# Kernel optimization log

Hardware: AMD Instinct MI355X
Metric: run time of the kernel (lower is better)

The kernel has to match this reference:

```python
import jax, jax.numpy as jnp
import numpy as np

N, E, G = 50000, 800000, 128
IN, HID, OUT, H = 128, 64, 32, 4
EPS = 1e-5


def _bn(x, g, b, m, v):
    # BatchNorm1d in eval mode: normalize with running stats
    return (x - m) * jax.lax.rsqrt(v + EPS) * g + b


def _gat(x, src, dst, W, att_src, att_dst, bias, n):
    # PyG GATConv, concat=False: mean over heads
    h = (x @ W).reshape(n, H, -1)                      # [N,H,C]
    a_src = (h * att_src).sum(-1)                      # [N,H]
    a_dst = (h * att_dst).sum(-1)                      # [N,H]
    e = jax.nn.leaky_relu(a_src[src] + a_dst[dst], 0.2)  # [E,H]
    m = jax.ops.segment_max(e, dst, num_segments=n)    # segment softmax over incoming edges
    e = jnp.exp(e - m[dst])
    s = jax.ops.segment_sum(e, dst, num_segments=n)
    alpha = e / s[dst]                                  # [E,H]
    out = jax.ops.segment_sum(alpha[:, :, None] * h[src], dst, num_segments=n)  # [N,H,C]
    return out.mean(axis=1) + bias


def setup_inputs() -> dict:
    key = jax.random.key(0)
    ks = jax.random.split(key, 20)
    d = {
        "x": jax.random.normal(ks[0], (N, IN), jnp.float32),
        "edge_index": jax.random.randint(ks[1], (2, E), 0, N),
        "batch": jnp.sort(jax.random.randint(ks[2], (N,), 0, G)),
        # input_norm
        "in_gamma": jax.random.normal(ks[3], (IN,)) * 0.05 + 1.0,
        "in_beta": jax.random.normal(ks[4], (IN,)) * 0.05,
        "in_mean": jax.random.normal(ks[5], (IN,)) * 0.05,
        "in_var": jax.random.uniform(ks[6], (IN,)) + 0.5,
        # gat1
        "W1": jax.random.normal(ks[7], (IN, H * HID)) * (1.0 / np.sqrt(IN)),
        "as1": jax.random.normal(ks[8], (H, HID)) * 0.1,
        "ad1": jax.random.normal(ks[9], (H, HID)) * 0.1,
        "b1": jnp.zeros((HID,)),
        "bn1_g": jnp.ones((HID,)),
        "bn1_b": jnp.zeros((HID,)),
        "bn1_m": jax.random.normal(ks[10], (HID,)) * 0.05,
        "bn1_v": jax.random.uniform(ks[11], (HID,)) + 0.5,
        # gat2
        "W2": jax.random.normal(ks[12], (HID, H * HID)) * (1.0 / np.sqrt(HID)),
        "as2": jax.random.normal(ks[13], (H, HID)) * 0.1,
        "ad2": jax.random.normal(ks[14], (H, HID)) * 0.1,
        "b2": jnp.zeros((HID,)),
        "bn2_g": jnp.ones((HID,)),
        "bn2_b": jnp.zeros((HID,)),
        "bn2_m": jax.random.normal(ks[15], (HID,)) * 0.05,
        "bn2_v": jax.random.uniform(ks[16], (HID,)) + 0.5,
        # head
        "fc1_w": jax.random.normal(ks[17], (HID, HID // 2)) * (1.0 / np.sqrt(HID)),
        "fc1_b": jnp.zeros((HID // 2,)),
        "fc2_w": jax.random.normal(ks[18], (HID // 2, OUT)) * (1.0 / np.sqrt(HID // 2)),
        "fc2_b": jnp.zeros((OUT,)),
    }
    return d


def reference(x, edge_index, batch, in_gamma, in_beta, in_mean, in_var,
              W1, as1, ad1, b1, bn1_g, bn1_b, bn1_m, bn1_v,
              W2, as2, ad2, b2, bn2_g, bn2_b, bn2_m, bn2_v,
              fc1_w, fc1_b, fc2_w, fc2_b):
    n = x.shape[0]
    # PyG GATConv adds self-loops by default
    loop = jnp.arange(n)
    src = jnp.concatenate([edge_index[0], loop])
    dst = jnp.concatenate([edge_index[1], loop])

    h = _bn(x, in_gamma, in_beta, in_mean, in_var)
    h = _gat(h, src, dst, W1, as1, ad1, b1, n)
    h = jax.nn.relu(_bn(h, bn1_g, bn1_b, bn1_m, bn1_v))
    # dropout p=0.3 is identity in eval mode
    h = _gat(h, src, dst, W2, as2, ad2, b2, n)
    h = jax.nn.relu(_bn(h, bn2_g, bn2_b, bn2_m, bn2_v))

    # global mean pool over graphs
    sums = jax.ops.segment_sum(h, batch, num_segments=G)
    cnts = jax.ops.segment_sum(jnp.ones((n,), h.dtype), batch, num_segments=G)
    emb = sums / jnp.maximum(cnts, 1.0)[:, None]

    out = jax.nn.relu(emb @ fc1_w + fc1_b)
    return out @ fc2_w + fc2_b
```

## Files before the change

### kernel.cpp

```cpp
#include <hip/hip_runtime.h>
#include <hip/hip_bf16.h>

#define EPS   1e-5f
#define NH    4
#define DIN   128
#define DHID  64
#define DOUT  32
#define PNODES 256
#define CAP   128
#define GM    32
#define NBUCK 64
#define BSTR  16
#define EPT   16
#define EPB   (256 * EPT)

typedef __attribute__((ext_vector_type(8))) short short8;
typedef __attribute__((ext_vector_type(4))) float f32x4;
typedef __attribute__((ext_vector_type(2))) float f32x2;

__device__ __forceinline__ float us2f(unsigned short u) {
    return __uint_as_float((unsigned)u << 16);
}
__device__ __forceinline__ unsigned short f2us(float v) {
    __hip_bfloat16 hb = __float2bfloat16(v);
    return *(unsigned short*)&hb;
}
__device__ __forceinline__ unsigned char f2e4m3(float v) {
    int p = __builtin_amdgcn_cvt_pk_fp8_f32(v, 0.f, 0, false);
    return (unsigned char)(p & 0xff);
}
__device__ __forceinline__ float lrelu(float a) { return (a >= 0.f) ? a : 0.2f * a; }

__global__ void k_init0(int* __restrict__ deg, float* __restrict__ pool,
                        int* __restrict__ bcur, int N, int npool) {
    int g = blockIdx.x * blockDim.x + threadIdx.x;
    if (g < N) deg[g] = 1;
    if (g < npool) pool[g] = 0.f;
    if (g < NBUCK * BSTR) bcur[g] = 0;
}

__global__ __launch_bounds__(256) void k_scan_a(const int* __restrict__ deg,
                                                int* __restrict__ rowptr,
                                                int* __restrict__ bsum, int N) {
    __shared__ int sh[256];
    const int t = threadIdx.x;
    const int i = blockIdx.x * 256 + t;
    int v = (i < N) ? deg[i] : 0;
    sh[t] = v;
    __syncthreads();
    #pragma unroll
    for (int o = 1; o < 256; o <<= 1) {
        int u = (t >= o) ? sh[t - o] : 0;
        __syncthreads();
        sh[t] += u;
        __syncthreads();
    }
    if (i < N) rowptr[i] = sh[t] - v;
    if (t == 255) bsum[blockIdx.x] = sh[255];
}

__global__ __launch_bounds__(256) void k_scan_b(int* __restrict__ bsum, int nb) {
    __shared__ int sh[256];
    const int t = threadIdx.x;
    int v = (t < nb) ? bsum[t] : 0;
    sh[t] = v;
    __syncthreads();
    #pragma unroll
    for (int o = 1; o < 256; o <<= 1) {
        int u = (t >= o) ? sh[t - o] : 0;
        __syncthreads();
        sh[t] += u;
        __syncthreads();
    }
    if (t < nb) bsum[t] = sh[t] - v;
}

__global__ __launch_bounds__(256) void k_scan_c(int* __restrict__ rowptr,
                                                int* __restrict__ cursor,
                                                const int* __restrict__ bsum,
                                                int N, int Etot) {
    const int i = blockIdx.x * 256 + threadIdx.x;
    if (i < N) {
        int v = rowptr[i] + bsum[blockIdx.x];
        rowptr[i] = v;
        cursor[i] = v;
    }
    if (i == 0) rowptr[N] = Etot;
}

__global__ __launch_bounds__(256) void k_part(
    const int* __restrict__ ei, int E, int N, int bshift,
    unsigned long long* __restrict__ arena, int* __restrict__ bcur,
    int* __restrict__ deg, int cap)
{
    __shared__ int lhist[NBUCK];
    __shared__ int lbase[NBUCK];
    const int t = threadIdx.x;
    const int e0 = blockIdx.x * EPB;
    const int eEnd = min(e0 + EPB, E + N);

    if (t < NBUCK) lhist[t] = 0;
    __syncthreads();

    int myb[EPT], myd[EPT], mys[EPT];
    #pragma unroll
    for (int r = 0; r < EPT; ++r) {
        int e = e0 + r * 256 + t;
        myb[r] = -1;
        if (e < eEnd) {
            int s, d;
            if (e < E) { s = ei[e]; d = ei[E + e]; atomicAdd(&deg[d], 1); }
            else       { s = d = e - E; }
            int b = d >> bshift;
            myb[r] = b; myd[r] = d; mys[r] = s;
            atomicAdd(&lhist[b], 1);
        }
    }
    __syncthreads();

    if (t < NBUCK) {
        int c = lhist[t];
        lbase[t] = c ? atomicAdd(&bcur[t * BSTR], c) : 0;
        lhist[t] = 0;
    }
    __syncthreads();

    #pragma unroll
    for (int r = 0; r < EPT; ++r) {
        int b = myb[r];
        if (b >= 0) {
            int li = atomicAdd(&lhist[b], 1);
            int pos = lbase[b] + li;
            if (pos >= cap) pos = cap - 1;
            arena[(size_t)b * cap + pos] =
                ((unsigned long long)(unsigned)myd[r] << 32) | (unsigned)mys[r];
        }
    }
}

__global__ __launch_bounds__(256) void k_fill2(
    const unsigned long long* __restrict__ arena, const int* __restrict__ bcur,
    int cap, int* __restrict__ cursor, int* __restrict__ col)
{
    const int b = blockIdx.x;
    const int idx = blockIdx.y * 256 + threadIdx.x;
    if (idx >= bcur[b * BSTR]) return;
    unsigned long long v = arena[(size_t)b * cap + idx];
    int d = (int)(v >> 32);
    int s = (int)(v & 0xffffffffu);
    int pos = atomicAdd(&cursor[d], 1);
    col[pos] = s;
}

__global__ __launch_bounds__(256) void k_prepw(
    const float* __restrict__ ing, const float* __restrict__ inb,
    const float* __restrict__ inm, const float* __restrict__ inv,
    const float* __restrict__ W1, const float* __restrict__ W2,
    const float* __restrict__ as1, const float* __restrict__ ad1,
    const float* __restrict__ as2, const float* __restrict__ ad2,
    const float* __restrict__ b1,
    const float* __restrict__ bn1g, const float* __restrict__ bn1b,
    const float* __restrict__ bn1m, const float* __restrict__ bn1v,
    unsigned short* __restrict__ Wt, unsigned short* __restrict__ Wt2,
    unsigned short* __restrict__ Wast1, unsigned short* __restrict__ Wast2,
    float* __restrict__ scl1, float* __restrict__ shf1,
    float* __restrict__ sclX, float* __restrict__ shfX)
{
    int g = blockIdx.x * blockDim.x + threadIdx.x;
    if (g < 256 * DIN) {
        int n = g >> 7, k = g & 127;
        Wt[g] = f2us(W1[(size_t)k * 256 + n]);
    }
    if (g < 256 * DHID) {
        int n = g >> 6, k = g & 63;
        Wt2[g] = f2us(W2[(size_t)k * 256 + n]);
    }
    if (g < 16 * DIN) {
        int c = g >> 7, k = g & 127;
        float s = 0.f;
        if (c < 4)      { for (int j = 0; j < 64; ++j) s += W1[(size_t)k * 256 + c * 64 + j] * as1[c * 64 + j]; }
        else if (c < 8) { for (int j = 0; j < 64; ++j) s += W1[(size_t)k * 256 + (c - 4) * 64 + j] * ad1[(c - 4) * 64 + j]; }
        Wast1[g] = f2us(s);
    }
    if (g < 16 * DHID) {
        int c = g >> 6, k = g & 63;
        float s = 0.f;
        if (c < 4)      { for (int j = 0; j < 64; ++j) s += W2[(size_t)k * 256 + c * 64 + j] * as2[c * 64 + j]; }
        else if (c < 8) { for (int j = 0; j < 64; ++j) s += W2[(size_t)k * 256 + (c - 4) * 64 + j] * ad2[(c - 4) * 64 + j]; }
        Wast2[g] = f2us(s);
    }
    if (g < DHID) {
        float sc = bn1g[g] * rsqrtf(bn1v[g] + EPS);
        scl1[g] = sc;
        shf1[g] = (b1[g] - bn1m[g]) * sc + bn1b[g];
    }
    if (g < DIN) {
        float sc = ing[g] * rsqrtf(inv[g] + EPS);
        sclX[g] = sc;
        shfX[g] = inb[g] - inm[g] * sc;
    }
}

__global__ __launch_bounds__(256) void k_gemm1(
    const float* __restrict__ x,
    const float* __restrict__ sclX, const float* __restrict__ shfX,
    const unsigned short* __restrict__ Wt,
    const unsigned short* __restrict__ Wast,
    unsigned char* __restrict__ h,
    float* __restrict__ asrc, float* __restrict__ adst, int N)
{
    __shared__ float Csh[GM][260];
    const int t = threadIdx.x;
    const int lane = t & 63, wv = t >> 6;
    const int qm = lane & 15, qd = lane >> 4;
    const int base = blockIdx.x * GM;

    short8 afr[2][4];
    #pragma unroll
    for (int ks = 0; ks < 4; ++ks) {
        const int k0 = qd * 8 + ks * 32;
        float4 s0 = *(const float4*)(sclX + k0), s1 = *(const float4*)(sclX + k0 + 4);
        float4 h0 = *(const float4*)(shfX + k0), h1 = *(const float4*)(shfX + k0 + 4);
        #pragma unroll
        for (int rt = 0; rt < 2; ++rt) {
            int node = base + rt * 16 + qm;
            if (node >= N) node = N - 1;
            const float* xp = x + (size_t)node * DIN + k0;
            float4 x0 = *(const float4*)xp, x1 = *(const float4*)(xp + 4);
            short8 v;
            v[0] = f2us(x0.x * s0.x + h0.x); v[1] = f2us(x0.y * s0.y + h0.y);
            v[2] = f2us(x0.z * s0.z + h0.z); v[3] = f2us(x0.w * s0.w + h0.w);
            v[4] = f2us(x1.x * s1.x + h1.x); v[5] = f2us(x1.y * s1.y + h1.y);
            v[6] = f2us(x1.z * s1.z + h1.z); v[7] = f2us(x1.w * s1.w + h1.w);
            afr[rt][ks] = v;
        }
    }

    const int n0 = wv * 64;
    f32x4 acc[2][4];
    #pragma unroll
    for (int rt = 0; rt < 2; ++rt)
        #pragma unroll
        for (int ct = 0; ct < 4; ++ct)
            acc[rt][ct] = (f32x4){0.f, 0.f, 0.f, 0.f};

    #pragma unroll
    for (int ct = 0; ct < 4; ++ct) {
        const unsigned short* bp = Wt + (size_t)(n0 + ct * 16 + qm) * DIN + qd * 8;
        #pragma unroll
        for (int ks = 0; ks < 4; ++ks) {
            short8 bfr = *(const short8*)(bp + ks * 32);
            acc[0][ct] = __builtin_amdgcn_mfma_f32_16x16x32_bf16(afr[0][ks], bfr, acc[0][ct], 0, 0, 0);
            acc[1][ct] = __builtin_amdgcn_mfma_f32_16x16x32_bf16(afr[1][ks], bfr, acc[1][ct], 0, 0, 0);
// ... 87 lines not shown
    {
        const unsigned short* wp = Wast + (size_t)qm * DHID + qd * 8;
        f32x4 aat[2];
        aat[0] = (f32x4){0.f, 0.f, 0.f, 0.f};
        aat[1] = (f32x4){0.f, 0.f, 0.f, 0.f};
        #pragma unroll
        for (int ks = 0; ks < 2; ++ks) {
            short8 wfr = *(const short8*)(wp + ks * 32);
            aat[0] = __builtin_amdgcn_mfma_f32_16x16x32_bf16(afr[0][ks], wfr, aat[0], 0, 0, 0);
            aat[1] = __builtin_amdgcn_mfma_f32_16x16x32_bf16(afr[1][ks], wfr, aat[1], 0, 0, 0);
        }
        const int c = qm;
        #pragma unroll
        for (int rt = 0; rt < 2; ++rt)
            #pragma unroll
            for (int rg = 0; rg < 4; ++rg) {
                int nd = base + rt * 16 + qd * 4 + rg;
                if (nd < N) {
                    if (c < 4)      asrc[nd * 4 + c] = aat[rt][rg];
                    else if (c < 8) adst[nd * 4 + (c - 4)] = aat[rt][rg];
                }
            }
    }

    #pragma unroll
    for (int rt = 0; rt < 2; ++rt)
        #pragma unroll
        for (int ct = 0; ct < 4; ++ct)
            #pragma unroll
            for (int rg = 0; rg < 4; ++rg)
                Csh[rt * 16 + qd * 4 + rg][n0 + ct * 16 + qm] = acc[rt][ct][rg];
    __syncthreads();

    const int hcol = ((t & 3) << 6) | (t >> 2);
    for (int r = 0; r < GM; ++r) {
        int node = base + r;
        if (node >= N) break;
        h[(size_t)node * 256 + t] = f2e4m3(Csh[r][hcol]);
    }
}

__global__ __launch_bounds__(256) void k_agg(
    const int* __restrict__ rowptr, const int* __restrict__ col,
    const float* __restrict__ asrc, const float* __restrict__ adst,
    const unsigned char* __restrict__ h8,
    float* __restrict__ outf, unsigned short* __restrict__ outb,
    const float* __restrict__ scl, const float* __restrict__ shf,
    int mode, int N)
{
    __shared__ float4 exs[4][CAP];
    __shared__ int    cols[4][CAP];
    const int lane = threadIdx.x & 63;
    const int wv   = threadIdx.x >> 6;
    const int d = (blockIdx.x << 2) + wv;
    if (d >= N) return;
    const int r0  = rowptr[d];
    const int deg = rowptr[d + 1] - r0;

    const float4 ad4 = ((const float4*)adst)[d];
    const float4* __restrict__ as4 = (const float4*)asrc;

    float sm0 = 0.f, sm1 = 0.f, sm2 = 0.f, sm3 = 0.f;
    for (int j = lane; j < deg; j += 64) {
        int s = col[r0 + j];
        float4 a = as4[s];
        float e0 = __expf(lrelu(a.x + ad4.x));
        float e1 = __expf(lrelu(a.y + ad4.y));
        float e2 = __expf(lrelu(a.z + ad4.z));
        float e3 = __expf(lrelu(a.w + ad4.w));
        if (j < CAP) { cols[wv][j] = s; exs[wv][j] = make_float4(e0, e1, e2, e3); }
        sm0 += e0; sm1 += e1; sm2 += e2; sm3 += e3;
    }
    #pragma unroll
    for (int o = 1; o < 64; o <<= 1) {
        sm0 += __shfl_xor(sm0, o, 64);
        sm1 += __shfl_xor(sm1, o, 64);
        sm2 += __shfl_xor(sm2, o, 64);
        sm3 += __shfl_xor(sm3, o, 64);
    }
    const float i0 = 0.25f / sm0, i1 = 0.25f / sm1, i2 = 0.25f / sm2, i3 = 0.25f / sm3;

    const unsigned int* __restrict__ hu = (const unsigned int*)h8;
    float a0 = 0.f, a1 = 0.f, a2 = 0.f, a3 = 0.f;
    float b0 = 0.f, b1 = 0.f, b2 = 0.f, b3 = 0.f;
    if (deg <= CAP) {
        int j = 0;
        for (; j + 3 < deg; j += 4) {
            int sA = cols[wv][j],     sB = cols[wv][j + 1];
            int sC = cols[wv][j + 2], sD = cols[wv][j + 3];
            unsigned int vA = hu[(size_t)sA * 64 + lane];
            unsigned int vB = hu[(size_t)sB * 64 + lane];
            unsigned int vC = hu[(size_t)sC * 64 + lane];
            unsigned int vD = hu[(size_t)sD * 64 + lane];
            float4 wA = exs[wv][j],     wB = exs[wv][j + 1];
            float4 wC = exs[wv][j + 2], wD = exs[wv][j + 3];
            f32x2 lA = __builtin_amdgcn_cvt_pk_f32_fp8(vA, false), hA = __builtin_amdgcn_cvt_pk_f32_fp8(vA, true);
            f32x2 lB = __builtin_amdgcn_cvt_pk_f32_fp8(vB, false), hB = __builtin_amdgcn_cvt_pk_f32_fp8(vB, true);
            f32x2 lC = __builtin_amdgcn_cvt_pk_f32_fp8(vC, false), hC = __builtin_amdgcn_cvt_pk_f32_fp8(vC, true);
            f32x2 lD = __builtin_amdgcn_cvt_pk_f32_fp8(vD, false), hD = __builtin_amdgcn_cvt_pk_f32_fp8(vD, true);
            a0 += wA.x * lA.x; a1 += wA.y * lA.y; a2 += wA.z * hA.x; a3 += wA.w * hA.y;
            b0 += wB.x * lB.x; b1 += wB.y * lB.y; b2 += wB.z * hB.x; b3 += wB.w * hB.y;
            a0 += wC.x * lC.x; a1 += wC.y * lC.y; a2 += wC.z * hC.x; a3 += wC.w * hC.y;
            b0 += wD.x * lD.x; b1 += wD.y * lD.y; b2 += wD.z * hD.x; b3 += wD.w * hD.y;
        }
        for (; j < deg; ++j) {
            int s = cols[wv][j];
            unsigned int v = hu[(size_t)s * 64 + lane];
            float4 w = exs[wv][j];
            f32x2 lo = __builtin_amdgcn_cvt_pk_f32_fp8(v, false), hi = __builtin_amdgcn_cvt_pk_f32_fp8(v, true);
            a0 += w.x * lo.x; a1 += w.y * lo.y; a2 += w.z * hi.x; a3 += w.w * hi.y;
        }
    } else {
        for (int j = 0; j < deg; ++j) {
            int s; float4 w;
            if (j < CAP) { s = cols[wv][j]; w = exs[wv][j]; }
            else {
                s = col[r0 + j];
                float4 a = as4[s];
                w.x = __expf(lrelu(a.x + ad4.x)); w.y = __expf(lrelu(a.y + ad4.y));
                w.z = __expf(lrelu(a.z + ad4.z)); w.w = __expf(lrelu(a.w + ad4.w));
            }
            unsigned int v = hu[(size_t)s * 64 + lane];
            f32x2 lo = __builtin_amdgcn_cvt_pk_f32_fp8(v, false), hi = __builtin_amdgcn_cvt_pk_f32_fp8(v, true);
            a0 += w.x * lo.x; a1 += w.y * lo.y; a2 += w.z * hi.x; a3 += w.w * hi.y;
        }
    }
    float acc = (a0 + b0) * i0 + (a1 + b1) * i1 + (a2 + b2) * i2 + (a3 + b3) * i3;

    if (mode) {
        float v = fmaxf(acc * scl[lane] + shf[lane], 0.f);
        outb[(size_t)d * 64 + lane] = f2us(v);
    } else {
        outf[(size_t)d * 64 + lane] = acc;
    }
}

__global__ __launch_bounds__(256) void k_pool(
    const float* __restrict__ outacc,
    const float* __restrict__ b2_,
    const float* __restrict__ bg, const float* __restrict__ bb,
    const float* __restrict__ bm, const float* __restrict__ bv,
    const int* __restrict__ batch,
    float* __restrict__ pool, float* __restrict__ cnt, int N)
{
    const int lane = threadIdx.x & 63;
    const int wave = threadIdx.x >> 6;
    const int base = blockIdx.x * PNODES;
    int end = base + PNODES; if (end > N) end = N;

    const float scale = bg[lane] * rsqrtf(bv[lane] + EPS);
    const float shift = (b2_[lane] - bm[lane]) * scale + bb[lane];

    float acc = 0.f;
    int cur = -1, cl = 0;
    for (int n = base + wave; n < end; n += 4) {
        int gr = batch[n];
        if (gr != cur) {
            if (cur >= 0) {
                atomicAdd(&pool[cur * 64 + lane], acc);
                if (lane == 0) atomicAdd(&cnt[cur], (float)cl);
            }
            cur = gr; acc = 0.f; cl = 0;
        }
        float v = fmaxf(outacc[(size_t)n * 64 + lane] * scale + shift, 0.f);
        acc += v; ++cl;
    }
    if (cur >= 0) {
        atomicAdd(&pool[cur * 64 + lane], acc);
        if (lane == 0) atomicAdd(&cnt[cur], (float)cl);
    }
}

__global__ void k_head(const float* __restrict__ pool, const float* __restrict__ cnt,
                       const float* __restrict__ fc1w, const float* __restrict__ fc1b,
                       const float* __restrict__ fc2w, const float* __restrict__ fc2b,
                       float* __restrict__ out)
{
    int g = blockIdx.x;
    int t = threadIdx.x;
    __shared__ float emb[64];
    __shared__ float z1[32];
    float c = fmaxf(cnt[g], 1.0f);
    emb[t] = pool[g * 64 + t] / c;
    __syncthreads();
    if (t < 32) {
        float s = fc1b[t];
        for (int k = 0; k < 64; ++k) s += emb[k] * fc1w[k * 32 + t];
        z1[t] = fmaxf(s, 0.f);
    }
    __syncthreads();
    if (t < 32) {
        float o = fc2b[t];
        for (int j = 0; j < 32; ++j) o += z1[j] * fc2w[j * 32 + t];
        out[g * 32 + t] = o;
    }
}

extern "C" void kernel_launch(void* const* d_in, const int* in_sizes, int n_in,
                              void* d_out, int out_size, void* d_ws, size_t ws_size,
                              hipStream_t stream)
{
    const float* x    = (const float*)d_in[0];
    const int*   ei   = (const int*)d_in[1];
    const int*   batch= (const int*)d_in[2];
    const float* ing  = (const float*)d_in[3];
    const float* inb  = (const float*)d_in[4];
    const float* inm  = (const float*)d_in[5];
    const float* inv  = (const float*)d_in[6];
    const float* W1   = (const float*)d_in[7];
    const float* as1  = (const float*)d_in[8];
    const float* ad1  = (const float*)d_in[9];
    const float* b1   = (const float*)d_in[10];
    const float* bn1g = (const float*)d_in[11];
    const float* bn1b = (const float*)d_in[12];
    const float* bn1m = (const float*)d_in[13];
    const float* bn1v = (const float*)d_in[14];
    const float* W2   = (const float*)d_in[15];
    const float* as2  = (const float*)d_in[16];
    const float* ad2  = (const float*)d_in[17];
    const float* b2   = (const float*)d_in[18];
    const float* bn2g = (const float*)d_in[19];
    const float* bn2b = (const float*)d_in[20];
    const float* bn2m = (const float*)d_in[21];
    const float* bn2v = (const float*)d_in[22];
    const float* fc1w = (const float*)d_in[23];
    const float* fc1b = (const float*)d_in[24];
    const float* fc2w = (const float*)d_in[25];
    const float* fc2b = (const float*)d_in[26];

    const int N = in_sizes[0] / DIN;
    const int E = in_sizes[1] / 2;
    const int G = out_size / DOUT;
    const int Etot = E + N;

    int bshift = 0;
    while ((N >> bshift) >= NBUCK) ++bshift;
    const int cap = (int)(((long long)Etot << bshift) / N * 5 / 4) + 512;

    unsigned char* h8 = (unsigned char*)d_ws;
    float* asrc   = (float*)(h8 + (size_t)N * 256);
    float* adst   = asrc + (size_t)N * NH;
    unsigned short* Wt    = (unsigned short*)(adst + (size_t)N * NH);
    unsigned short* Wt2   = Wt + 256 * DIN;
    unsigned short* Wast1 = Wt2 + 256 * DHID;
    unsigned short* Wast2 = Wast1 + 16 * DIN;
    float* scl1   = (float*)(Wast2 + 16 * DHID);
    float* shf1   = scl1 + DHID;
    float* sclX   = shf1 + DHID;
    float* shfX   = sclX + DIN;
    float* outacc = shfX + DIN;
    unsigned short* A2 = (unsigned short*)outacc;
    int*   deg    = (int*)(outacc + (size_t)N * DHID);
    int*   rowptr = deg + N;
    int*   cursor = rowptr + N + 1;
    int*   col    = cursor + N;
    float* pool   = (float*)(col + Etot);
    float* cnt    = pool + (size_t)G * DHID;
    int*   bsum   = (int*)(cnt + G);
    int*   bcur   = (int*)(((size_t)(bsum + 256) + 63) & ~(size_t)63);
    unsigned long long* arena =
        (unsigned long long*)(((size_t)(bcur + NBUCK * BSTR) + 7) & ~(size_t)7);

    const int npool = G * DHID + G;
    const int nScanBlk = (N + 255) / 256;
    dim3 b256(256);

    k_init0<<<(N + 255) / 256, b256, 0, stream>>>(deg, pool, bcur, N, npool);
    k_part<<<(Etot + EPB - 1) / EPB, b256, 0, stream>>>(ei, E, N, bshift, arena, bcur, deg, cap);
    k_scan_a<<<nScanBlk, b256, 0, stream>>>(deg, rowptr, bsum, N);
    k_scan_b<<<1, b256, 0, stream>>>(bsum, nScanBlk);
    k_scan_c<<<nScanBlk, b256, 0, stream>>>(rowptr, cursor, bsum, N, Etot);
    {
        dim3 gFill(NBUCK, (cap + 255) / 256);
        k_fill2<<<gFill, b256, 0, stream>>>(arena, bcur, cap, cursor, col);
    }

    k_prepw<<<(256 * DIN + 255) / 256, b256, 0, stream>>>(
        ing, inb, inm, inv, W1, W2, as1, ad1, as2, ad2,
        b1, bn1g, bn1b, bn1m, bn1v,
        Wt, Wt2, Wast1, Wast2, scl1, shf1, sclX, shfX);

    k_gemm1<<<(N + GM - 1) / GM, b256, 0, stream>>>(x, sclX, shfX, Wt, Wast1, h8, asrc, adst, N);
    k_agg<<<(N + 3) / 4, b256, 0, stream>>>(rowptr, col, asrc, adst, h8,
                                            (float*)nullptr, A2, scl1, shf1, 1, N);

    k_gemm2<<<(N + GM - 1) / GM, b256, 0, stream>>>(A2, Wt2, Wast2, h8, asrc, adst, N);
    k_agg<<<(N + 3) / 4, b256, 0, stream>>>(rowptr, col, asrc, adst, h8,
                                            outacc, (unsigned short*)nullptr,
                                            (const float*)nullptr, (const float*)nullptr, 0, N);

    k_pool<<<(N + PNODES - 1) / PNODES, b256, 0, stream>>>(outacc, b2, bn2g, bn2b, bn2m, bn2v,
                                                           batch, pool, cnt, N);
    k_head<<<G, 64, 0, stream>>>(pool, cnt, fc1w, fc1b, fc2w, fc2b, (float*)d_out);
}
```

Before: 364.4 us.

## Handle self-loops implicitly, merge init/prep kernels, use 16-byte gathers in aggregation

Self-loop edges are no longer stored in the CSR. Each destination's self term is computed directly in the aggregation kernel and appended to the per-wave shared edge list. The init and weight-prep kernels are fused into one setup kernel to cut a launch. The aggregation gather is reorganized so 16-lane groups each load a full 256-byte fp8 row with uint4 loads, processing four edges per iteration and reducing across groups with shuffles; this widens memory transactions at the cost of more registers and a cross-group reduction.

```diff
diff --git a/kernel.cpp b/kernel.cpp
--- a/kernel.cpp
+++ b/kernel.cpp
@@ -31,128 +31,9 @@
 }
 __device__ __forceinline__ float lrelu(float a) { return (a >= 0.f) ? a : 0.2f * a; }
 
-__global__ void k_init0(int* __restrict__ deg, float* __restrict__ pool,
-                        int* __restrict__ bcur, int N, int npool) {
-    int g = blockIdx.x * blockDim.x + threadIdx.x;
-    if (g < N) deg[g] = 1;
-    if (g < npool) pool[g] = 0.f;
-    if (g < NBUCK * BSTR) bcur[g] = 0;
-}
-
-__global__ __launch_bounds__(256) void k_scan_a(const int* __restrict__ deg,
-                                                int* __restrict__ rowptr,
-                                                int* __restrict__ bsum, int N) {
-    __shared__ int sh[256];
-    const int t = threadIdx.x;
-    const int i = blockIdx.x * 256 + t;
-    int v = (i < N) ? deg[i] : 0;
-    sh[t] = v;
-    __syncthreads();
-    #pragma unroll
-    for (int o = 1; o < 256; o <<= 1) {
-        int u = (t >= o) ? sh[t - o] : 0;
-        __syncthreads();
-        sh[t] += u;
-        __syncthreads();
-    }
-    if (i < N) rowptr[i] = sh[t] - v;
-    if (t == 255) bsum[blockIdx.x] = sh[255];
-}
-
-__global__ __launch_bounds__(256) void k_scan_b(int* __restrict__ bsum, int nb) {
-    __shared__ int sh[256];
-    const int t = threadIdx.x;
-    int v = (t < nb) ? bsum[t] : 0;
-    sh[t] = v;
-    __syncthreads();
-    #pragma unroll
-    for (int o = 1; o < 256; o <<= 1) {
-        int u = (t >= o) ? sh[t - o] : 0;
-        __syncthreads();
-        sh[t] += u;
-        __syncthreads();
-    }
-    if (t < nb) bsum[t] = sh[t] - v;
-}
-
-__global__ __launch_bounds__(256) void k_scan_c(int* __restrict__ rowptr,
-                                                int* __restrict__ cursor,
-                                                const int* __restrict__ bsum,
-                                                int N, int Etot) {
-    const int i = blockIdx.x * 256 + threadIdx.x;
-    if (i < N) {
-        int v = rowptr[i] + bsum[blockIdx.x];
-        rowptr[i] = v;
-        cursor[i] = v;
-    }
-    if (i == 0) rowptr[N] = Etot;
-}
-
-__global__ __launch_bounds__(256) void k_part(
-    const int* __restrict__ ei, int E, int N, int bshift,
-    unsigned long long* __restrict__ arena, int* __restrict__ bcur,
-    int* __restrict__ deg, int cap)
-{
-    __shared__ int lhist[NBUCK];
-    __shared__ int lbase[NBUCK];
-    const int t = threadIdx.x;
-    const int e0 = blockIdx.x * EPB;
-    const int eEnd = min(e0 + EPB, E + N);
-
-    if (t < NBUCK) lhist[t] = 0;
-    __syncthreads();
-
-    int myb[EPT], myd[EPT], mys[EPT];
-    #pragma unroll
-    for (int r = 0; r < EPT; ++r) {
-        int e = e0 + r * 256 + t;
-        myb[r] = -1;
-        if (e < eEnd) {
-            int s, d;
-            if (e < E) { s = ei[e]; d = ei[E + e]; atomicAdd(&deg[d], 1); }
-            else       { s = d = e - E; }
-            int b = d >> bshift;
-            myb[r] = b; myd[r] = d; mys[r] = s;
-            atomicAdd(&lhist[b], 1);
-        }
-    }
-    __syncthreads();
-
-    if (t < NBUCK) {
-        int c = lhist[t];
-        lbase[t] = c ? atomicAdd(&bcur[t * BSTR], c) : 0;
-        lhist[t] = 0;
-    }
-    __syncthreads();
-
-    #pragma unroll
-    for (int r = 0; r < EPT; ++r) {
-        int b = myb[r];
-        if (b >= 0) {
-            int li = atomicAdd(&lhist[b], 1);
-            int pos = lbase[b] + li;
-            if (pos >= cap) pos = cap - 1;
-            arena[(size_t)b * cap + pos] =
-                ((unsigned long long)(unsigned)myd[r] << 32) | (unsigned)mys[r];
-        }
-    }
-}
-
-__global__ __launch_bounds__(256) void k_fill2(
-    const unsigned long long* __restrict__ arena, const int* __restrict__ bcur,
-    int cap, int* __restrict__ cursor, int* __restrict__ col)
-{
-    const int b = blockIdx.x;
-    const int idx = blockIdx.y * 256 + threadIdx.x;
-    if (idx >= bcur[b * BSTR]) return;
-    unsigned long long v = arena[(size_t)b * cap + idx];
-    int d = (int)(v >> 32);
-    int s = (int)(v & 0xffffffffu);
-    int pos = atomicAdd(&cursor[d], 1);
-    col[pos] = s;
-}
-
-__global__ __launch_bounds__(256) void k_prepw(
+__global__ __launch_bounds__(256) void k_setup(
+    int* __restrict__ deg, float* __restrict__ pool, int* __restrict__ bcur,
+    int N, int npool,
     const float* __restrict__ ing, const float* __restrict__ inb,
     const float* __restrict__ inm, const float* __restrict__ inv,
     const float* __restrict__ W1, const float* __restrict__ W2,
@@ -167,6 +48,9 @@
     float* __restrict__ sclX, float* __restrict__ shfX)
 {
     int g = blockIdx.x * blockDim.x + threadIdx.x;
+    if (g < N) deg[g] = 0;
+    if (g < npool) pool[g] = 0.f;
+    if (g < NBUCK * BSTR) bcur[g] = 0;
     if (g < 256 * DIN) {
         int n = g >> 7, k = g & 127;
         Wt[g] = f2us(W1[(size_t)k * 256 + n]);
@@ -199,6 +83,118 @@
         sclX[g] = sc;
         shfX[g] = inb[g] - inm[g] * sc;
     }
+}
+
+__global__ __launch_bounds__(256) void k_scan_a(const int* __restrict__ deg,
+                                                int* __restrict__ rowptr,
+                                                int* __restrict__ bsum, int N) {
+    __shared__ int sh[256];
+    const int t = threadIdx.x;
+    const int i = blockIdx.x * 256 + t;
+    int v = (i < N) ? deg[i] : 0;
+    sh[t] = v;
+    __syncthreads();
+    #pragma unroll
+    for (int o = 1; o < 256; o <<= 1) {
+        int u = (t >= o) ? sh[t - o] : 0;
+        __syncthreads();
+        sh[t] += u;
+        __syncthreads();
+    }
+    if (i < N) rowptr[i] = sh[t] - v;
+    if (t == 255) bsum[blockIdx.x] = sh[255];
+}
+
+__global__ __launch_bounds__(256) void k_scan_b(int* __restrict__ bsum, int nb) {
+    __shared__ int sh[256];
+    const int t = threadIdx.x;
+    int v = (t < nb) ? bsum[t] : 0;
+    sh[t] = v;
+    __syncthreads();
+    #pragma unroll
+    for (int o = 1; o < 256; o <<= 1) {
+        int u = (t >= o) ? sh[t - o] : 0;
+        __syncthreads();
+        sh[t] += u;
+        __syncthreads();
+    }
+    if (t < nb) bsum[t] = sh[t] - v;
+}
+
+__global__ __launch_bounds__(256) void k_scan_c(int* __restrict__ rowptr,
+                                                int* __restrict__ cursor,
+                                                const int* __restrict__ bsum,
+                                                int N, int Etot) {
+    const int i = blockIdx.x * 256 + threadIdx.x;
+    if (i < N) {
+        int v = rowptr[i] + bsum[blockIdx.x];
+        rowptr[i] = v;
+        cursor[i] = v;
+    }
+    if (i == 0) rowptr[N] = Etot;
+}
+
+__global__ __launch_bounds__(256) void k_part(
+    const int* __restrict__ ei, int E, int bshift,
+    unsigned long long* __restrict__ arena, int* __restrict__ bcur,
+    int* __restrict__ deg, int cap)
+{
+    __shared__ int lhist[NBUCK];
+    __shared__ int lbase[NBUCK];
+    const int t = threadIdx.x;
+    const int e0 = blockIdx.x * EPB;
+    const int eEnd = min(e0 + EPB, E);
+
+    if (t < NBUCK) lhist[t] = 0;
+    __syncthreads();
+
+    int myb[EPT], myd[EPT], mys[EPT];
+    #pragma unroll
+    for (int r = 0; r < EPT; ++r) {
+        int e = e0 + r * 256 + t;
+        myb[r] = -1;
+        if (e < eEnd) {
+            int s = ei[e], d = ei[E + e];
+            atomicAdd(&deg[d], 1);
+            int b = d >> bshift;
+            myb[r] = b; myd[r] = d; mys[r] = s;
+            atomicAdd(&lhist[b], 1);
+        }
+    }
+    __syncthreads();
+
+    if (t < NBUCK) {
+        int c = lhist[t];
+        lbase[t] = c ? atomicAdd(&bcur[t * BSTR], c) : 0;
+        lhist[t] = 0;
+    }
+    __syncthreads();
+
+    #pragma unroll
+    for (int r = 0; r < EPT; ++r) {
+        int b = myb[r];
+        if (b >= 0) {
+            int li = atomicAdd(&lhist[b], 1);
+            int pos = lbase[b] + li;
+            if (pos >= cap) pos = cap - 1;
+            arena[(size_t)b * cap + pos] =
+                ((unsigned long long)(unsigned)myd[r] << 32) | (unsigned)mys[r];
+        }
+    }
+}
+
+__global__ __launch_bounds__(256) void k_fill2(
+    const unsigned long long* __restrict__ arena, const int* __restrict__ bcur,
+    int cap, int* __restrict__ cursor, int* __restrict__ col)
+{
+    const int b = blockIdx.x;
+    const int idx = blockIdx.y * 256 + threadIdx.x;
+    if (idx >= bcur[b * BSTR]) return;
+    unsigned long long v = arena[(size_t)b * cap + idx];
+    int d = (int)(v >> 32);
+    int s = (int)(v & 0xffffffffu);
+    int pos = atomicAdd(&cursor[d], 1);
+    col[pos] = s;
 }
 
 __global__ __launch_bounds__(256) void k_gemm1(
@@ -392,13 +388,22 @@
     __shared__ int    cols[4][CAP];
     const int lane = threadIdx.x & 63;
     const int wv   = threadIdx.x >> 6;
+    const int grp  = lane >> 4;
+    const int l16  = lane & 15;
     const int d = (blockIdx.x << 2) + wv;
     if (d >= N) return;
     const int r0  = rowptr[d];
     const int deg = rowptr[d + 1] - r0;
+    const int degv = deg + 1;
 
     const float4 ad4 = ((const float4*)adst)[d];
     const float4* __restrict__ as4 = (const float4*)asrc;
+
+    const float4 a_s = as4[d];
+    const float ws0 = __expf(lrelu(a_s.x + ad4.x));
+    const float ws1 = __expf(lrelu(a_s.y + ad4.y));
+    const float ws2 = __expf(lrelu(a_s.z + ad4.z));
+    const float ws3 = __expf(lrelu(a_s.w + ad4.w));
 
     float sm0 = 0.f, sm1 = 0.f, sm2 = 0.f, sm3 = 0.f;
     for (int j = lane; j < deg; j += 64) {
@@ -418,60 +423,119 @@
         sm2 += __shfl_xor(sm2, o, 64);
         sm3 += __shfl_xor(sm3, o, 64);
     }
+    sm0 += ws0; sm1 += ws1; sm2 += ws2; sm3 += ws3;
     const float i0 = 0.25f / sm0, i1 = 0.25f / sm1, i2 = 0.25f / sm2, i3 = 0.25f / sm3;
 
-    const unsigned int* __restrict__ hu = (const unsigned int*)h8;
-    float a0 = 0.f, a1 = 0.f, a2 = 0.f, a3 = 0.f;
-    float b0 = 0.f, b1 = 0.f, b2 = 0.f, b3 = 0.f;
-    if (deg <= CAP) {
-        int j = 0;
-        for (; j + 3 < deg; j += 4) {
-            int sA = cols[wv][j],     sB = cols[wv][j + 1];
-            int sC = cols[wv][j + 2], sD = cols[wv][j + 3];
-            unsigned int vA = hu[(size_t)sA * 64 + lane];
-            unsigned int vB = hu[(size_t)sB * 64 + lane];
-            unsigned int vC = hu[(size_t)sC * 64 + lane];
-            unsigned int vD = hu[(size_t)sD * 64 + lane];
-            float4 wA = exs[wv][j],     wB = exs[wv][j + 1];
-            float4 wC = exs[wv][j + 2], wD = exs[wv][j + 3];
-            f32x2 lA = __builtin_amdgcn_cvt_pk_f32_fp8(vA, false), hA = __builtin_amdgcn_cvt_pk_f32_fp8(vA, true);
-            f32x2 lB = __builtin_amdgcn_cvt_pk_f32_fp8(vB, false), hB = __builtin_amdgcn_cvt_pk_f32_fp8(vB, true);
-            f32x2 lC = __builtin_amdgcn_cvt_pk_f32_fp8(vC, false), hC = __builtin_amdgcn_cvt_pk_f32_fp8(vC, true);
-            f32x2 lD = __builtin_amdgcn_cvt_pk_f32_fp8(vD, false), hD = __builtin_amdgcn_cvt_pk_f32_fp8(vD, true);
-            a0 += wA.x * lA.x; a1 += wA.y * lA.y; a2 += wA.z * hA.x; a3 += wA.w * hA.y;
-            b0 += wB.x * lB.x; b1 += wB.y * lB.y; b2 += wB.z * hB.x; b3 += wB.w * hB.y;
-            a0 += wC.x * lC.x; a1 += wC.y * lC.y; a2 += wC.z * hC.x; a3 += wC.w * hC.y;
-            b0 += wD.x * lD.x; b1 += wD.y * lD.y; b2 += wD.z * hD.x; b3 += wD.w * hD.y;
-        }
-        for (; j < deg; ++j) {
-            int s = cols[wv][j];
-            unsigned int v = hu[(size_t)s * 64 + lane];
-            float4 w = exs[wv][j];
-            f32x2 lo = __builtin_amdgcn_cvt_pk_f32_fp8(v, false), hi = __builtin_amdgcn_cvt_pk_f32_fp8(v, true);
-            a0 += w.x * lo.x; a1 += w.y * lo.y; a2 += w.z * hi.x; a3 += w.w * hi.y;
+    if (deg < CAP && lane == 0) {
+        cols[wv][deg] = d;
+        exs[wv][deg] = make_float4(ws0, ws1, ws2, ws3);
+    }
+
+    float acc[4][4];
+    #pragma unroll
+    for (int i = 0; i < 4; ++i)
+        #pragma unroll
+        for (int hh = 0; hh < 4; ++hh) acc[i][hh] = 0.f;
+
+    if (degv <= CAP) {
+        for (int j = 0; j < degv; j += 4) {
+            int e = j + grp;
+            int s = d;
+            float4 w = make_float4(0.f, 0.f, 0.f, 0.f);
+            if (e < degv) { s = cols[wv][e]; w = exs[wv][e]; }
+            uint4 v4 = *(const uint4*)(h8 + (size_t)s * 256 + l16 * 16);
+            {
+                f32x2 lo = __builtin_amdgcn_cvt_pk_f32_fp8(v4.x, false);
+                f32x2 hi = __builtin_amdgcn_cvt_pk_f32_fp8(v4.x, true);
+                acc[0][0] += w.x * lo.x; acc[0][1] += w.y * lo.y;
+                acc[0][2] += w.z * hi.x; acc[0][3] += w.w * hi.y;
+            }
+            {
+                f32x2 lo = __builtin_amdgcn_cvt_pk_f32_fp8(v4.y, false);
+                f32x2 hi = __builtin_amdgcn_cvt_pk_f32_fp8(v4.y, true);
+                acc[1][0] += w.x * lo.x; acc[1][1] += w.y * lo.y;
+                acc[1][2] += w.z * hi.x; acc[1][3] += w.w * hi.y;
+            }
+            {
+                f32x2 lo = __builtin_amdgcn_cvt_pk_f32_fp8(v4.z, false);
+                f32x2 hi = __builtin_amdgcn_cvt_pk_f32_fp8(v4.z, true);
+                acc[2][0] += w.x * lo.x; acc[2][1] += w.y * lo.y;
+                acc[2][2] += w.z * hi.x; acc[2][3] += w.w * hi.y;
+            }
+            {
+                f32x2 lo = __builtin_amdgcn_cvt_pk_f32_fp8(v4.w, false);
+                f32x2 hi = __builtin_amdgcn_cvt_pk_f32_fp8(v4.w, true);
+                acc[3][0] += w.x * lo.x; acc[3][1] += w.y * lo.y;
+                acc[3][2] += w.z * hi.x; acc[3][3] += w.w * hi.y;
+            }
         }
     } else {
-        for (int j = 0; j < deg; ++j) {
-            int s; float4 w;
-            if (j < CAP) { s = cols[wv][j]; w = exs[wv][j]; }
-            else {
-                s = col[r0 + j];
+        for (int j = 0; j < degv; j += 4) {
+            int e = j + grp;
+            int s = d;
+            float4 w = make_float4(0.f, 0.f, 0.f, 0.f);
+            if (e < CAP)      { s = cols[wv][e]; w = exs[wv][e]; }
+            else if (e < deg) {
+                s = col[r0 + e];
                 float4 a = as4[s];
                 w.x = __expf(lrelu(a.x + ad4.x)); w.y = __expf(lrelu(a.y + ad4.y));
                 w.z = __expf(lrelu(a.z + ad4.z)); w.w = __expf(lrelu(a.w + ad4.w));
             }
-            unsigned int v = hu[(size_t)s * 64 + lane];
-            f32x2 lo = __builtin_amdgcn_cvt_pk_f32_fp8(v, false), hi = __builtin_amdgcn_cvt_pk_f32_fp8(v, true);
-            a0 += w.x * lo.x; a1 += w.y * lo.y; a2 += w.z * hi.x; a3 += w.w * hi.y;
-        }
-    }
-    float acc = (a0 + b0) * i0 + (a1 + b1) * i1 + (a2 + b2) * i2 + (a3 + b3) * i3;
-
-    if (mode) {
-        float v = fmaxf(acc * scl[lane] + shf[lane], 0.f);
-        outb[(size_t)d * 64 + lane] = f2us(v);
-    } else {
-        outf[(size_t)d * 64 + lane] = acc;
+            else if (e == deg) { s = d; w = make_float4(ws0, ws1, ws2, ws3); }
+            uint4 v4 = *(const uint4*)(h8 + (size_t)s * 256 + l16 * 16);
+            {
+                f32x2 lo = __builtin_amdgcn_cvt_pk_f32_fp8(v4.x, false);
+                f32x2 hi = __builtin_amdgcn_cvt_pk_f32_fp8(v4.x, true);
+                acc[0][0] += w.x * lo.x; acc[0][1] += w.y * lo.y;
+                acc[0][2] += w.z * hi.x; acc[0][3] += w.w * hi.y;
+            }
+            {
+                f32x2 lo = __builtin_amdgcn_cvt_pk_f32_fp8(v4.y, false);
+                f32x2 hi = __builtin_amdgcn_cvt_pk_f32_fp8(v4.y, true);
+                acc[1][0] += w.x * lo.x; acc[1][1] += w.y * lo.y;
+                acc[1][2] += w.z * hi.x; acc[1][3] += w.w * hi.y;
+            }
+            {
+                f32x2 lo = __builtin_amdgcn_cvt_pk_f32_fp8(v4.z, false);
+                f32x2 hi = __builtin_amdgcn_cvt_pk_f32_fp8(v4.z, true);
+                acc[2][0] += w.x * lo.x; acc[2][1] += w.y * lo.y;
+                acc[2][2] += w.z * hi.x; acc[2][3] += w.w * hi.y;
+            }
+            {
+                f32x2 lo = __builtin_amdgcn_cvt_pk_f32_fp8(v4.w, false);
+                f32x2 hi = __builtin_amdgcn_cvt_pk_f32_fp8(v4.w, true);
+                acc[3][0] += w.x * lo.x; acc[3][1] += w.y * lo.y;
+                acc[3][2] += w.z * hi.x; acc[3][3] += w.w * hi.y;
+            }
+        }
+    }
+
+    float4 r;
+    {
+        float v0 = acc[0][0] * i0 + acc[0][1] * i1 + acc[0][2] * i2 + acc[0][3] * i3;
+        float v1 = acc[1][0] * i0 + acc[1][1] * i1 + acc[1][2] * i2 + acc[1][3] * i3;
+        float v2 = acc[2][0] * i0 + acc[2][1] * i1 + acc[2][2] * i2 + acc[2][3] * i3;
+        float v3 = acc[3][0] * i0 + acc[3][1] * i1 + acc[3][2] * i2 + acc[3][3] * i3;
+        v0 += __shfl_xor(v0, 16, 64); v0 += __shfl_xor(v0, 32, 64);
+        v1 += __shfl_xor(v1, 16, 64); v1 += __shfl_xor(v1, 32, 64);
+        v2 += __shfl_xor(v2, 16, 64); v2 += __shfl_xor(v2, 32, 64);
+        v3 += __shfl_xor(v3, 16, 64); v3 += __shfl_xor(v3, 32, 64);
+        r = make_float4(v0, v1, v2, v3);
+    }
+    if (grp == 0) {
+        const int c0 = l16 * 4;
+        if (mode) {
+            float4 sc = *(const float4*)(scl + c0);
+            float4 sf = *(const float4*)(shf + c0);
+            ushort4 o;
+            o.x = f2us(fmaxf(r.x * sc.x + sf.x, 0.f));
+            o.y = f2us(fmaxf(r.y * sc.y + sf.y, 0.f));
+            o.z = f2us(fmaxf(r.z * sc.z + sf.z, 0.f));
+            o.w = f2us(fmaxf(r.w * sc.w + sf.w, 0.f));
+            *(ushort4*)(outb + (size_t)d * 64 + c0) = o;
+        } else {
+            *(float4*)(outf + (size_t)d * 64 + c0) = r;
+        }
     }
 }
 
@@ -571,11 +635,10 @@
     const int N = in_sizes[0] / DIN;
     const int E = in_sizes[1] / 2;
     const int G = out_size / DOUT;
-    const int Etot = E + N;
 
     int bshift = 0;
     while ((N >> bshift) >= NBUCK) ++bshift;
-    const int cap = (int)(((long long)Etot << bshift) / N * 5 / 4) + 512;
+    const int cap = (int)(((long long)E << bshift) / N * 5 / 4) + 512;
 
     unsigned char* h8 = (unsigned char*)d_ws;
     float* asrc   = (float*)(h8 + (size_t)N * 256);
@@ -594,7 +657,7 @@
     int*   rowptr = deg + N;
     int*   cursor = rowptr + N + 1;
     int*   col    = cursor + N;
-    float* pool   = (float*)(col + Etot);
+    float* pool   = (float*)(col + E);
     float* cnt    = pool + (size_t)G * DHID;
     int*   bsum   = (int*)(cnt + G);
     int*   bcur   = (int*)(((size_t)(bsum + 256) + 63) & ~(size_t)63);
@@ -605,20 +668,23 @@
     const int nScanBlk = (N + 255) / 256;
     dim3 b256(256);
 
-    k_init0<<<(N + 255) / 256, b256, 0, stream>>>(deg, pool, bcur, N, npool);
-    k_part<<<(Etot + EPB - 1) / EPB, b256, 0, stream>>>(ei, E, N, bshift, arena, bcur, deg, cap);
+    int setupTot = N;
+    if (setupTot < npool) setupTot = npool;
+    if (setupTot < 256 * DIN) setupTot = 256 * DIN;
+    k_setup<<<(setupTot + 255) / 256, b256, 0, stream>>>(
+        deg, pool, bcur, N, npool,
+        ing, inb, inm, inv, W1, W2, as1, ad1, as2, ad2,
+        b1, bn1g, bn1b, bn1m, bn1v,
+        Wt, Wt2, Wast1, Wast2, scl1, shf1, sclX, shfX);
+
+    k_part<<<(E + EPB - 1) / EPB, b256, 0, stream>>>(ei, E, bshift, arena, bcur, deg, cap);
     k_scan_a<<<nScanBlk, b256, 0, stream>>>(deg, rowptr, bsum, N);
     k_scan_b<<<1, b256, 0, stream>>>(bsum, nScanBlk);
-    k_scan_c<<<nScanBlk, b256, 0, stream>>>(rowptr, cursor, bsum, N, Etot);
+    k_scan_c<<<nScanBlk, b256, 0, stream>>>(rowptr, cursor, bsum, N, E);
     {
         dim3 gFill(NBUCK, (cap + 255) / 256);
         k_fill2<<<gFill, b256, 0, stream>>>(arena, bcur, cap, cursor, col);
     }
-
-    k_prepw<<<(256 * DIN + 255) / 256, b256, 0, stream>>>(
-        ing, inb, inm, inv, W1, W2, as1, ad1, as2, ad2,
-        b1, bn1g, bn1b, bn1m, bn1v,
-        Wt, Wt2, Wast1, Wast2, scl1, shf1, sclX, shfX);
 
     k_gemm1<<<(N + GM - 1) / GM, b256, 0, stream>>>(x, sclX, shfX, Wt, Wast1, h8, asrc, adst, N);
     k_agg<<<(N + 3) / 4, b256, 0, stream>>>(rowptr, col, asrc, adst, h8,
```

Measured after the change: 373.5 us. 1.03x slower.

## Handle self-loops implicitly in aggregation and merge init with weight prep

Applied to the files above, without the earlier changes.

Self-loop edges are no longer built into the CSR. Degrees start at zero, the partition, scan and fill steps handle only the E real edges, and each aggregation wave computes the self-loop weight directly and appends it to its shared-memory neighbor list. The init kernel is also folded into the weight-preparation kernel, which removes one launch. This trims N entries from the CSR build and its atomics, in exchange for extra per-node work and extra branches in the aggregation kernel.

```diff
diff --git a/kernel.cpp b/kernel.cpp
--- a/kernel.cpp
+++ b/kernel.cpp
@@ -31,128 +31,9 @@
 }
 __device__ __forceinline__ float lrelu(float a) { return (a >= 0.f) ? a : 0.2f * a; }
 
-__global__ void k_init0(int* __restrict__ deg, float* __restrict__ pool,
-                        int* __restrict__ bcur, int N, int npool) {
-    int g = blockIdx.x * blockDim.x + threadIdx.x;
-    if (g < N) deg[g] = 1;
-    if (g < npool) pool[g] = 0.f;
-    if (g < NBUCK * BSTR) bcur[g] = 0;
-}
-
-__global__ __launch_bounds__(256) void k_scan_a(const int* __restrict__ deg,
-                                                int* __restrict__ rowptr,
-                                                int* __restrict__ bsum, int N) {
-    __shared__ int sh[256];
-    const int t = threadIdx.x;
-    const int i = blockIdx.x * 256 + t;
-    int v = (i < N) ? deg[i] : 0;
-    sh[t] = v;
-    __syncthreads();
-    #pragma unroll
-    for (int o = 1; o < 256; o <<= 1) {
-        int u = (t >= o) ? sh[t - o] : 0;
-        __syncthreads();
-        sh[t] += u;
-        __syncthreads();
-    }
-    if (i < N) rowptr[i] = sh[t] - v;
-    if (t == 255) bsum[blockIdx.x] = sh[255];
-}
-
-__global__ __launch_bounds__(256) void k_scan_b(int* __restrict__ bsum, int nb) {
-    __shared__ int sh[256];
-    const int t = threadIdx.x;
-    int v = (t < nb) ? bsum[t] : 0;
-    sh[t] = v;
-    __syncthreads();
-    #pragma unroll
-    for (int o = 1; o < 256; o <<= 1) {
-        int u = (t >= o) ? sh[t - o] : 0;
-        __syncthreads();
-        sh[t] += u;
-        __syncthreads();
-    }
-    if (t < nb) bsum[t] = sh[t] - v;
-}
-
-__global__ __launch_bounds__(256) void k_scan_c(int* __restrict__ rowptr,
-                                                int* __restrict__ cursor,
-                                                const int* __restrict__ bsum,
-                                                int N, int Etot) {
-    const int i = blockIdx.x * 256 + threadIdx.x;
-    if (i < N) {
-        int v = rowptr[i] + bsum[blockIdx.x];
-        rowptr[i] = v;
-        cursor[i] = v;
-    }
-    if (i == 0) rowptr[N] = Etot;
-}
-
-__global__ __launch_bounds__(256) void k_part(
-    const int* __restrict__ ei, int E, int N, int bshift,
-    unsigned long long* __restrict__ arena, int* __restrict__ bcur,
-    int* __restrict__ deg, int cap)
-{
-    __shared__ int lhist[NBUCK];
-    __shared__ int lbase[NBUCK];
-    const int t = threadIdx.x;
-    const int e0 = blockIdx.x * EPB;
-    const int eEnd = min(e0 + EPB, E + N);
-
-    if (t < NBUCK) lhist[t] = 0;
-    __syncthreads();
-
-    int myb[EPT], myd[EPT], mys[EPT];
-    #pragma unroll
-    for (int r = 0; r < EPT; ++r) {
-        int e = e0 + r * 256 + t;
-        myb[r] = -1;
-        if (e < eEnd) {
-            int s, d;
-            if (e < E) { s = ei[e]; d = ei[E + e]; atomicAdd(&deg[d], 1); }
-            else       { s = d = e - E; }
-            int b = d >> bshift;
-            myb[r] = b; myd[r] = d; mys[r] = s;
-            atomicAdd(&lhist[b], 1);
-        }
-    }
-    __syncthreads();
-
-    if (t < NBUCK) {
-        int c = lhist[t];
-        lbase[t] = c ? atomicAdd(&bcur[t * BSTR], c) : 0;
-        lhist[t] = 0;
-    }
-    __syncthreads();
-
-    #pragma unroll
-    for (int r = 0; r < EPT; ++r) {
-        int b = myb[r];
-        if (b >= 0) {
-            int li = atomicAdd(&lhist[b], 1);
-            int pos = lbase[b] + li;
-            if (pos >= cap) pos = cap - 1;
-            arena[(size_t)b * cap + pos] =
-                ((unsigned long long)(unsigned)myd[r] << 32) | (unsigned)mys[r];
-        }
-    }
-}
-
-__global__ __launch_bounds__(256) void k_fill2(
-    const unsigned long long* __restrict__ arena, const int* __restrict__ bcur,
-    int cap, int* __restrict__ cursor, int* __restrict__ col)
-{
-    const int b = blockIdx.x;
-    const int idx = blockIdx.y * 256 + threadIdx.x;
-    if (idx >= bcur[b * BSTR]) return;
-    unsigned long long v = arena[(size_t)b * cap + idx];
-    int d = (int)(v >> 32);
-    int s = (int)(v & 0xffffffffu);
-    int pos = atomicAdd(&cursor[d], 1);
-    col[pos] = s;
-}
-
-__global__ __launch_bounds__(256) void k_prepw(
+__global__ __launch_bounds__(256) void k_setup(
+    int* __restrict__ deg, float* __restrict__ pool, int* __restrict__ bcur,
+    int N, int npool,
     const float* __restrict__ ing, const float* __restrict__ inb,
     const float* __restrict__ inm, const float* __restrict__ inv,
     const float* __restrict__ W1, const float* __restrict__ W2,
@@ -167,6 +48,9 @@
     float* __restrict__ sclX, float* __restrict__ shfX)
 {
     int g = blockIdx.x * blockDim.x + threadIdx.x;
+    if (g < N) deg[g] = 0;
+    if (g < npool) pool[g] = 0.f;
+    if (g < NBUCK * BSTR) bcur[g] = 0;
     if (g < 256 * DIN) {
         int n = g >> 7, k = g & 127;
         Wt[g] = f2us(W1[(size_t)k * 256 + n]);
@@ -199,6 +83,118 @@
         sclX[g] = sc;
         shfX[g] = inb[g] - inm[g] * sc;
     }
+}
+
+__global__ __launch_bounds__(256) void k_scan_a(const int* __restrict__ deg,
+                                                int* __restrict__ rowptr,
+                                                int* __restrict__ bsum, int N) {
+    __shared__ int sh[256];
+    const int t = threadIdx.x;
+    const int i = blockIdx.x * 256 + t;
+    int v = (i < N) ? deg[i] : 0;
+    sh[t] = v;
+    __syncthreads();
+    #pragma unroll
+    for (int o = 1; o < 256; o <<= 1) {
+        int u = (t >= o) ? sh[t - o] : 0;
+        __syncthreads();
+        sh[t] += u;
+        __syncthreads();
+    }
+    if (i < N) rowptr[i] = sh[t] - v;
+    if (t == 255) bsum[blockIdx.x] = sh[255];
+}
+
+__global__ __launch_bounds__(256) void k_scan_b(int* __restrict__ bsum, int nb) {
+    __shared__ int sh[256];
+    const int t = threadIdx.x;
+    int v = (t < nb) ? bsum[t] : 0;
+    sh[t] = v;
+    __syncthreads();
+    #pragma unroll
+    for (int o = 1; o < 256; o <<= 1) {
+        int u = (t >= o) ? sh[t - o] : 0;
+        __syncthreads();
+        sh[t] += u;
+        __syncthreads();
+    }
+    if (t < nb) bsum[t] = sh[t] - v;
+}
+
+__global__ __launch_bounds__(256) void k_scan_c(int* __restrict__ rowptr,
+                                                int* __restrict__ cursor,
+                                                const int* __restrict__ bsum,
+                                                int N, int Etot) {
+    const int i = blockIdx.x * 256 + threadIdx.x;
+    if (i < N) {
+        int v = rowptr[i] + bsum[blockIdx.x];
+        rowptr[i] = v;
+        cursor[i] = v;
+    }
+    if (i == 0) rowptr[N] = Etot;
+}
+
+__global__ __launch_bounds__(256) void k_part(
+    const int* __restrict__ ei, int E, int bshift,
+    unsigned long long* __restrict__ arena, int* __restrict__ bcur,
+    int* __restrict__ deg, int cap)
+{
+    __shared__ int lhist[NBUCK];
+    __shared__ int lbase[NBUCK];
+    const int t = threadIdx.x;
+    const int e0 = blockIdx.x * EPB;
+    const int eEnd = min(e0 + EPB, E);
+
+    if (t < NBUCK) lhist[t] = 0;
+    __syncthreads();
+
+    int myb[EPT], myd[EPT], mys[EPT];
+    #pragma unroll
+    for (int r = 0; r < EPT; ++r) {
+        int e = e0 + r * 256 + t;
+        myb[r] = -1;
+        if (e < eEnd) {
+            int s = ei[e], d = ei[E + e];
+            atomicAdd(&deg[d], 1);
+            int b = d >> bshift;
+            myb[r] = b; myd[r] = d; mys[r] = s;
+            atomicAdd(&lhist[b], 1);
+        }
+    }
+    __syncthreads();
+
+    if (t < NBUCK) {
+        int c = lhist[t];
+        lbase[t] = c ? atomicAdd(&bcur[t * BSTR], c) : 0;
+        lhist[t] = 0;
+    }
+    __syncthreads();
+
+    #pragma unroll
+    for (int r = 0; r < EPT; ++r) {
+        int b = myb[r];
+        if (b >= 0) {
+            int li = atomicAdd(&lhist[b], 1);
+            int pos = lbase[b] + li;
+            if (pos >= cap) pos = cap - 1;
+            arena[(size_t)b * cap + pos] =
+                ((unsigned long long)(unsigned)myd[r] << 32) | (unsigned)mys[r];
+        }
+    }
+}
+
+__global__ __launch_bounds__(256) void k_fill2(
+    const unsigned long long* __restrict__ arena, const int* __restrict__ bcur,
+    int cap, int* __restrict__ cursor, int* __restrict__ col)
+{
+    const int b = blockIdx.x;
+    const int idx = blockIdx.y * 256 + threadIdx.x;
+    if (idx >= bcur[b * BSTR]) return;
+    unsigned long long v = arena[(size_t)b * cap + idx];
+    int d = (int)(v >> 32);
+    int s = (int)(v & 0xffffffffu);
+    int pos = atomicAdd(&cursor[d], 1);
+    col[pos] = s;
 }
 
 __global__ __launch_bounds__(256) void k_gemm1(
@@ -396,9 +392,16 @@
     if (d >= N) return;
     const int r0  = rowptr[d];
     const int deg = rowptr[d + 1] - r0;
+    const int degv = deg + 1;
 
     const float4 ad4 = ((const float4*)adst)[d];
     const float4* __restrict__ as4 = (const float4*)asrc;
+
+    const float4 a_s = as4[d];
+    const float ws0 = __expf(lrelu(a_s.x + ad4.x));
+    const float ws1 = __expf(lrelu(a_s.y + ad4.y));
+    const float ws2 = __expf(lrelu(a_s.z + ad4.z));
+    const float ws3 = __expf(lrelu(a_s.w + ad4.w));
 
     float sm0 = 0.f, sm1 = 0.f, sm2 = 0.f, sm3 = 0.f;
     for (int j = lane; j < deg; j += 64) {
@@ -418,14 +421,20 @@
         sm2 += __shfl_xor(sm2, o, 64);
         sm3 += __shfl_xor(sm3, o, 64);
     }
+    sm0 += ws0; sm1 += ws1; sm2 += ws2; sm3 += ws3;
     const float i0 = 0.25f / sm0, i1 = 0.25f / sm1, i2 = 0.25f / sm2, i3 = 0.25f / sm3;
+
+    if (deg < CAP && lane == 0) {
+        cols[wv][deg] = d;
+        exs[wv][deg] = make_float4(ws0, ws1, ws2, ws3);
+    }
 
     const unsigned int* __restrict__ hu = (const unsigned int*)h8;
     float a0 = 0.f, a1 = 0.f, a2 = 0.f, a3 = 0.f;
     float b0 = 0.f, b1 = 0.f, b2 = 0.f, b3 = 0.f;
-    if (deg <= CAP) {
+    if (degv <= CAP) {
         int j = 0;
-        for (; j + 3 < deg; j += 4) {
+        for (; j + 3 < degv; j += 4) {
             int sA = cols[wv][j],     sB = cols[wv][j + 1];
             int sC = cols[wv][j + 2], sD = cols[wv][j + 3];
             unsigned int vA = hu[(size_t)sA * 64 + lane];
@@ -443,7 +452,7 @@
             a0 += wC.x * lC.x; a1 += wC.y * lC.y; a2 += wC.z * hC.x; a3 += wC.w * hC.y;
             b0 += wD.x * lD.x; b1 += wD.y * lD.y; b2 += wD.z * hD.x; b3 += wD.w * hD.y;
         }
-        for (; j < deg; ++j) {
+        for (; j < degv; ++j) {
             int s = cols[wv][j];
             unsigned int v = hu[(size_t)s * 64 + lane];
             float4 w = exs[wv][j];
@@ -451,15 +460,16 @@
             a0 += w.x * lo.x; a1 += w.y * lo.y; a2 += w.z * hi.x; a3 += w.w * hi.y;
         }
     } else {
-        for (int j = 0; j < deg; ++j) {
+        for (int j = 0; j < degv; ++j) {
             int s; float4 w;
-            if (j < CAP) { s = cols[wv][j]; w = exs[wv][j]; }
-            else {
+            if (j < CAP)      { s = cols[wv][j]; w = exs[wv][j]; }
+            else if (j < deg) {
                 s = col[r0 + j];
                 float4 a = as4[s];
                 w.x = __expf(lrelu(a.x + ad4.x)); w.y = __expf(lrelu(a.y + ad4.y));
                 w.z = __expf(lrelu(a.z + ad4.z)); w.w = __expf(lrelu(a.w + ad4.w));
             }
+            else { s = d; w = make_float4(ws0, ws1, ws2, ws3); }
             unsigned int v = hu[(size_t)s * 64 + lane];
             f32x2 lo = __builtin_amdgcn_cvt_pk_f32_fp8(v, false), hi = __builtin_amdgcn_cvt_pk_f32_fp8(v, true);
             a0 += w.x * lo.x; a1 += w.y * lo.y; a2 += w.z * hi.x; a3 += w.w * hi.y;
@@ -571,11 +581,10 @@
     const int N = in_sizes[0] / DIN;
     const int E = in_sizes[1] / 2;
     const int G = out_size / DOUT;
-    const int Etot = E + N;
 
     int bshift = 0;
     while ((N >> bshift) >= NBUCK) ++bshift;
-    const int cap = (int)(((long long)Etot << bshift) / N * 5 / 4) + 512;
+    const int cap = (int)(((long long)E << bshift) / N * 5 / 4) + 512;
 
     unsigned char* h8 = (unsigned char*)d_ws;
     float* asrc   = (float*)(h8 + (size_t)N * 256);
@@ -594,7 +603,7 @@
     int*   rowptr = deg + N;
     int*   cursor = rowptr + N + 1;
     int*   col    = cursor + N;
-    float* pool   = (float*)(col + Etot);
+    float* pool   = (float*)(col + E);
     float* cnt    = pool + (size_t)G * DHID;
     int*   bsum   = (int*)(cnt + G);
     int*   bcur   = (int*)(((size_t)(bsum + 256) + 63) & ~(size_t)63);
@@ -605,20 +614,23 @@
     const int nScanBlk = (N + 255) / 256;
     dim3 b256(256);
 
-    k_init0<<<(N + 255) / 256, b256, 0, stream>>>(deg, pool, bcur, N, npool);
-    k_part<<<(Etot + EPB - 1) / EPB, b256, 0, stream>>>(ei, E, N, bshift, arena, bcur, deg, cap);
+    int setupTot = N;
+    if (setupTot < npool) setupTot = npool;
+    if (setupTot < 256 * DIN) setupTot = 256 * DIN;
+    k_setup<<<(setupTot + 255) / 256, b256, 0, stream>>>(
+        deg, pool, bcur, N, npool,
+        ing, inb, inm, inv, W1, W2, as1, ad1, as2, ad2,
+        b1, bn1g, bn1b, bn1m, bn1v,
+        Wt, Wt2, Wast1, Wast2, scl1, shf1, sclX, shfX);
+
+    k_part<<<(E + EPB - 1) / EPB, b256, 0, stream>>>(ei, E, bshift, arena, bcur, deg, cap);
     k_scan_a<<<nScanBlk, b256, 0, stream>>>(deg, rowptr, bsum, N);
     k_scan_b<<<1, b256, 0, stream>>>(bsum, nScanBlk);
-    k_scan_c<<<nScanBlk, b256, 0, stream>>>(rowptr, cursor, bsum, N, Etot);
+    k_scan_c<<<nScanBlk, b256, 0, stream>>>(rowptr, cursor, bsum, N, E);
     {
         dim3 gFill(NBUCK, (cap + 255) / 256);
         k_fill2<<<gFill, b256, 0, stream>>>(arena, bcur, cap, cursor, col);
     }
-
-    k_prepw<<<(256 * DIN + 255) / 256, b256, 0, stream>>>(
-        ing, inb, inm, inv, W1, W2, as1, ad1, as2, ad2,
-        b1, bn1g, bn1b, bn1m, bn1v,
-        Wt, Wt2, Wast1, Wast2, scl1, shf1, sclX, shfX);
 
     k_gemm1<<<(N + GM - 1) / GM, b256, 0, stream>>>(x, sclX, shfX, Wt, Wast1, h8, asrc, adst, N);
     k_agg<<<(N + 3) / 4, b256, 0, stream>>>(rowptr, col, asrc, adst, h8,
```

After: 374.3 us. 2.7% more time.
